# Optimization experiments

Measured on AMD Instinct MI355X. Metric: run time of the kernel, lower is better.

The kernel has to match this reference:

```python
import jax, jax.numpy as jnp
import numpy as np

N = 50000      # nodes
E = 800000     # directed edges (avg degree 16)
M = 10000      # hyperedges
P = 200000     # hypergraph incidence pairs (~4 per vertex)
D_IN = 64
D_OUT = 64
NEG_SLOPE = 0.2


def setup_inputs() -> dict:
    key = jax.random.key(0)
    ks = jax.random.split(key, 9)
    X = jax.random.normal(ks[0], (N, D_IN), jnp.float32)
    theta_w = jax.random.normal(ks[1], (D_OUT, D_IN), jnp.float32) / np.float32(np.sqrt(D_IN))
    theta_b = jax.random.normal(ks[2], (D_OUT,), jnp.float32) * 0.01
    a_src = jax.random.normal(ks[3], (D_OUT,), jnp.float32) / np.float32(np.sqrt(D_OUT))
    a_dst = jax.random.normal(ks[4], (D_OUT,), jnp.float32) / np.float32(np.sqrt(D_OUT))
    e_src = jax.random.randint(ks[5], (E,), 0, N, jnp.int32)
    e_dst = jax.random.randint(ks[6], (E,), 0, N, jnp.int32)
    inc_v = jax.random.randint(ks[7], (P,), 0, N, jnp.int32)
    inc_e = jax.random.randint(ks[8], (P,), 0, M, jnp.int32)
    return {"X": X, "theta_w": theta_w, "theta_b": theta_b, "a_src": a_src,
            "a_dst": a_dst, "e_src": e_src, "e_dst": e_dst,
            "inc_v": inc_v, "inc_e": inc_e}


def reference(X, theta_w, theta_b, a_src, a_dst, e_src, e_dst, inc_v, inc_e):
    # theta: Linear(in, out)
    Xp = X @ theta_w.T + theta_b                      # [N, D_OUT]
    # atten_src/atten_dst: Linear(out, 1, bias=False) -> per-node scalars
    s_src = Xp @ a_src                                # [N]
    s_dst = Xp @ a_dst                                # [N]
    # edge attention scores: gather + leaky_relu (dropout = identity in eval)
    score = jax.nn.leaky_relu(s_src[e_src] + s_dst[e_dst], NEG_SLOPE)  # [E]
    # segment softmax over incoming edges of each destination node
    seg_max = jax.ops.segment_max(score, e_dst, num_segments=N)
    seg_max = jax.lax.stop_gradient(jnp.where(jnp.isfinite(seg_max), seg_max, 0.0))
    w = jnp.exp(score - seg_max[e_dst])               # [E]
    denom = jax.ops.segment_sum(w, e_dst, num_segments=N)
    w = w / denom[e_dst]
    # weighted scatter-sum of source features (g.v2v softmax_then_sum)
    X_g = jax.ops.segment_sum(w[:, None] * Xp[e_src], e_dst, num_segments=N)
    # HGNN smoothing: D_v^{-1/2} H D_e^{-1} H^T D_v^{-1/2} Xp  (unit hyperedge weights)
    ones_p = jnp.ones((P,), Xp.dtype)
    dv = jax.ops.segment_sum(ones_p, inc_v, num_segments=N)
    de = jax.ops.segment_sum(ones_p, inc_e, num_segments=M)
    dv_isqrt = jnp.where(dv > 0, jax.lax.rsqrt(jnp.maximum(dv, 1.0)), 0.0)
    de_inv = jnp.where(de > 0, 1.0 / jnp.maximum(de, 1.0), 0.0)
    Xs = Xp * dv_isqrt[:, None]                        # [N, D_OUT]
    He = jax.ops.segment_sum(Xs[inc_v], inc_e, num_segments=M) * de_inv[:, None]  # [M, D_OUT]
    X_hg = jax.ops.segment_sum(He[inc_e], inc_v, num_segments=N) * dv_isqrt[:, None]
    X1 = (X_g + X_hg) * 0.5
    return jax.nn.elu(X1)
```

## Files before the change

kernel.cpp:

```cpp
#include <hip/hip_runtime.h>
#include <math.h>

#define DD 64

typedef __attribute__((ext_vector_type(8))) short bf16x8;
typedef __attribute__((ext_vector_type(4))) float f32x4;

__device__ __forceinline__ unsigned short f2bf(float x) {
    unsigned int u = __float_as_uint(x);
    u += 0x7fffu + ((u >> 16) & 1u);
    return (unsigned short)(u >> 16);
}
__device__ __forceinline__ float bflo(unsigned int u) { return __uint_as_float(u << 16); }
__device__ __forceinline__ float bfhi(unsigned int u) { return __uint_as_float(u & 0xffff0000u); }

#define GEMM_BLOCKS 196

__global__ __launch_bounds__(256) void k_gemm_count(
    const float* __restrict__ X, const float* __restrict__ W,
    const float* __restrict__ bias, const float* __restrict__ a_src,
    const float* __restrict__ a_dst, unsigned short* __restrict__ Xp_bf,
    float* __restrict__ s_src, float* __restrict__ s_dst,
    const int* __restrict__ e_dst, const int* __restrict__ inc_e,
    const int* __restrict__ inc_v, int* __restrict__ hist_g,
    int* __restrict__ hist_ie, int* __restrict__ hist_iv,
    int N, int E, int P, int M)
{
    if (blockIdx.x >= GEMM_BLOCKS) {
        __shared__ int cnt[128];
        int b = blockIdx.x - GEMM_BLOCKS;
        const int* key; int n, B, SH, nblk, blk; int* hist;
        if (b < 256)      { key = e_dst; n = E; B = (N + 511) >> 9; SH = 9; nblk = 256; blk = b;       hist = hist_g;  }
        else if (b < 384) { key = inc_e; n = P; B = (M + 255) >> 8; SH = 8; nblk = 128; blk = b - 256; hist = hist_ie; }
        else              { key = inc_v; n = P; B = (N + 511) >> 9; SH = 9; nblk = 128; blk = b - 384; hist = hist_iv; }
        for (int i = threadIdx.x; i < B; i += 256) cnt[i] = 0;
        __syncthreads();
        int chunk = (n + nblk - 1) / nblk;
        int s = blk * chunk, e = min(n, s + chunk);
        for (int i = s + threadIdx.x; i < e; i += 256)
            atomicAdd(&cnt[key[i] >> SH], 1);
        __syncthreads();
        for (int i = threadIdx.x; i < B; i += 256)
            hist[i * nblk + blk] = cnt[i];
        return;
    }
    int t = threadIdx.x;
    int lane = t & 63;
    int col = lane & 15;
    int kq  = lane >> 4;
    int rowbase = kq * 4;

    bf16x8 bfrag[4][2];
    float bj[4], asr[4], adr[4];
    #pragma unroll
    for (int jt = 0; jt < 4; ++jt) {
        int j = jt * 16 + col;
        #pragma unroll
        for (int ks = 0; ks < 2; ++ks) {
            const float* wp = W + j * DD + ks * 32 + kq * 8;
            float4 w0 = *(const float4*)wp;
            float4 w1 = *(const float4*)(wp + 4);
            bf16x8 bb;
            bb[0] = (short)f2bf(w0.x); bb[1] = (short)f2bf(w0.y);
            bb[2] = (short)f2bf(w0.z); bb[3] = (short)f2bf(w0.w);
            bb[4] = (short)f2bf(w1.x); bb[5] = (short)f2bf(w1.y);
            bb[6] = (short)f2bf(w1.z); bb[7] = (short)f2bf(w1.w);
            bfrag[jt][ks] = bb;
        }
        bj[jt]  = bias[j];
        asr[jt] = a_src[j];
        adr[jt] = a_dst[j];
    }

    int wave  = (blockIdx.x * 256 + t) >> 6;
    int nwave = (GEMM_BLOCKS * 256) >> 6;
    int ntiles = (N + 15) >> 4;
    for (int tile = wave; tile < ntiles; tile += nwave) {
        int r0 = tile * 16;
        int rl = r0 + col;
        if (rl >= N) rl = N - 1;
        const float* xp = X + (size_t)rl * DD + kq * 8;
        float4 x0 = *(const float4*)xp;
        float4 x1 = *(const float4*)(xp + 4);
        float4 x2 = *(const float4*)(xp + 32);
        float4 x3 = *(const float4*)(xp + 36);
        bf16x8 a0, a1;
        a0[0] = (short)f2bf(x0.x); a0[1] = (short)f2bf(x0.y);
        a0[2] = (short)f2bf(x0.z); a0[3] = (short)f2bf(x0.w);
        a0[4] = (short)f2bf(x1.x); a0[5] = (short)f2bf(x1.y);
        a0[6] = (short)f2bf(x1.z); a0[7] = (short)f2bf(x1.w);
        a1[0] = (short)f2bf(x2.x); a1[1] = (short)f2bf(x2.y);
        a1[2] = (short)f2bf(x2.z); a1[3] = (short)f2bf(x2.w);
        a1[4] = (short)f2bf(x3.x); a1[5] = (short)f2bf(x3.y);
        a1[6] = (short)f2bf(x3.z); a1[7] = (short)f2bf(x3.w);

        f32x4 acc[4];
        #pragma unroll
        for (int jt = 0; jt < 4; ++jt) {
            f32x4 c = {bj[jt], bj[jt], bj[jt], bj[jt]};
            c = __builtin_amdgcn_mfma_f32_16x16x32_bf16(a0, bfrag[jt][0], c, 0, 0, 0);
            c = __builtin_amdgcn_mfma_f32_16x16x32_bf16(a1, bfrag[jt][1], c, 0, 0, 0);
            acc[jt] = c;
        }

        int orow = r0 + rowbase;
        #pragma unroll
        for (int jt = 0; jt < 4; ++jt) {
            #pragma unroll
            for (int r = 0; r < 4; ++r) {
                int rr = orow + r;
                if (rr < N)
                    Xp_bf[(size_t)rr * DD + jt * 16 + col] = f2bf(acc[jt][r]);
            }
        }

        float vs[4], vd[4];
        #pragma unroll
        for (int r = 0; r < 4; ++r) {
            vs[r] = acc[0][r] * asr[0] + acc[1][r] * asr[1]
                  + acc[2][r] * asr[2] + acc[3][r] * asr[3];
            vd[r] = acc[0][r] * adr[0] + acc[1][r] * adr[1]
                  + acc[2][r] * adr[2] + acc[3][r] * adr[3];
        }
        #pragma unroll
        for (int off = 1; off < 16; off <<= 1) {
            #pragma unroll
            for (int r = 0; r < 4; ++r) {
                vs[r] += __shfl_xor(vs[r], off, 64);
                vd[r] += __shfl_xor(vd[r], off, 64);
            }
        }
        if (col == 0) {
            #pragma unroll
            for (int r = 0; r < 4; ++r) {
                int rr = orow + r;
                if (rr < N) { s_src[rr] = vs[r]; s_dst[rr] = vd[r]; }
            }
        }
    }
}

__device__ void block_scan4(int* a, int len)
{
    __shared__ int wtot[16];
    __shared__ int carry_s;
    int tid = threadIdx.x, lane = tid & 63, wid = tid >> 6;
    if (tid == 0) carry_s = 0;
    __syncthreads();
    for (int base = 0; base < len; base += 4096) {
        int i0 = base + tid * 4;
        int v[4];
        #pragma unroll
        for (int k = 0; k < 4; ++k) { int i = i0 + k; v[k] = (i < len) ? a[i] : 0; }
        int s = v[0] + v[1] + v[2] + v[3];
        int incl = s;
        #pragma unroll
        for (int off = 1; off < 64; off <<= 1) {
            int t = __shfl_up(incl, off, 64);
            if (lane >= off) incl += t;
        }
        if (lane == 63) wtot[wid] = incl;
        __syncthreads();
        int carry = carry_s;
        int woff = 0;
        for (int wj = 0; wj < wid; ++wj) woff += wtot[wj];
        int excl = carry + woff + incl - s;
        int run = excl;
        #pragma unroll
        for (int k = 0; k < 4; ++k) { int i = i0 + k; if (i < len) a[i] = run; run += v[k]; }
        __syncthreads();
        if (tid == 1023) carry_s = run;
        __syncthreads();
    }
    if (tid == 0) a[len] = carry_s;
}

__global__ __launch_bounds__(1024) void k_scan3(
    int* h0, int l0, int* h1, int l1, int* h2, int l2)
{
    if (blockIdx.x == 0)      block_scan4(h0, l0);
    else if (blockIdx.x == 1) block_scan4(h1, l1);
    else                      block_scan4(h2, l2);
}

__global__ __launch_bounds__(256) void k_scat(
    const int* __restrict__ e_dst, const int* __restrict__ e_src,
    const int* __restrict__ inc_e, const int* __restrict__ inc_v,
    const int* __restrict__ hist_g, const int* __restrict__ hist_ie,
    const int* __restrict__ hist_iv,
    unsigned int* __restrict__ pg, unsigned int* __restrict__ pie,
    unsigned int* __restrict__ piv,
    int E, int P, int N, int M)
{
    __shared__ int cur[128];
    int b = blockIdx.x;
    const int *key, *pay, *base; unsigned int* out;
    int n, B, SH, nblk, blk;
    if (b < 256)      { key = e_dst; pay = e_src; n = E; B = (N + 511) >> 9; SH = 9; nblk = 256; blk = b;       base = hist_g;  out = pg;  }
    else if (b < 384) { key = inc_e; pay = inc_v; n = P; B = (M + 255) >> 8; SH = 8; nblk = 128; blk = b - 256; base = hist_ie; out = pie; }
    else              { key = inc_v; pay = inc_e; n = P; B = (N + 511) >> 9; SH = 9; nblk = 128; blk = b - 384; base = hist_iv; out = piv; }
    for (int i = threadIdx.x; i < B; i += 256) cur[i] = base[i * nblk + blk];
    __syncthreads();
    int chunk = (n + nblk - 1) / nblk;
    int s = blk * chunk, e = min(n, s + chunk);
    int mask = (1 << SH) - 1;
    for (int i = s + threadIdx.x; i < e; i += 256) {
        int k = key[i];
        int pos = atomicAdd(&cur[k >> SH], 1);
        out[pos] = (unsigned int)(k & mask) | ((unsigned int)pay[i] << SH);
    }
}

__global__ __launch_bounds__(256) void k_fine(
    const int* __restrict__ hist_g, const int* __restrict__ hist_ie,
    const int* __restrict__ hist_iv,
    const unsigned int* __restrict__ pg, const unsigned int* __restrict__ pie,
    const unsigned int* __restrict__ piv,
    int* __restrict__ src_sorted, int* __restrict__ v_sorted,
    int* __restrict__ e_sorted,
    int* __restrict__ start_g, int* __restrict__ start_e,
    int* __restrict__ start_v,
    float* __restrict__ dein, float* __restrict__ dvis, int N, int M)
{
    __shared__ int lh[513];
    __shared__ int lc[512];
    __shared__ int lwt[4];
    __shared__ int lout[10240];
    int Bg = (N + 511) >> 9, Bie = (M + 255) >> 8;
    int b = blockIdx.x, tid = threadIdx.x;
    const int* base; const unsigned int* pr; int* outp; int* startp; float* inv;
    int K, nblk, b0, NK, mode;
    if (b < Bg)            { base = hist_g;  pr = pg;  outp = src_sorted; startp = start_g; inv = nullptr; K = 512; nblk = 256; b0 = b;            NK = N; mode = 0; }
    else if (b < Bg + Bie) { base = hist_ie; pr = pie; outp = v_sorted;   startp = start_e; inv = dein;    K = 256; nblk = 128; b0 = b - Bg;       NK = M; mode = 2; }
    else                   { base = hist_iv; pr = piv; outp = e_sorted;   startp = start_v; inv = dvis;    K = 512; nblk = 128; b0 = b - Bg - Bie; NK = N; mode = 1; }
    int SHF = (K == 512) ? 9 : 8;

    int pbase = base[b0 * nblk], pend = base[(b0 + 1) * nblk];
    int cnt = pend - pbase;
    for (int i = tid; i < K; i += 256) { lh[i] = 0; lc[i] = 0; }
    __syncthreads();
    for (int i = tid; i < cnt; i += 256)
        atomicAdd(&lh[pr[pbase + i] & (K - 1)], 1);
    __syncthreads();

    int per = K >> 8;
    int i0 = tid * per;
    int a0 = lh[i0], a1 = (per == 2) ? lh[i0 + 1] : 0;
    int ssum = a0 + a1;
    int lane = tid & 63, wid = tid >> 6;
    int incl = ssum;
    #pragma unroll
    for (int off = 1; off < 64; off <<= 1) {
        int t = __shfl_up(incl, off, 64);
        if (lane >= off) incl += t;
    }
    if (lane == 63) lwt[wid] = incl;
    __syncthreads();
    int woff = 0;
    for (int wj = 0; wj < wid; ++wj) woff += lwt[wj];
    int excl = woff + incl - ssum;
    lh[i0] = excl;
    if (per == 2) lh[i0 + 1] = excl + a0;
    if (tid == 255) lh[K] = excl + ssum;
    __syncthreads();

    for (int i = tid; i < cnt; i += 256) {
        unsigned int q = pr[pbase + i];
        int kl = q & (K - 1);
        int pos = lh[kl] + atomicAdd(&lc[kl], 1);
        lout[pos < 10240 ? pos : 10239] = (int)(q >> SHF);
    }
    __syncthreads();
    for (int i = tid; i < cnt; i += 256)
        outp[pbase + i] = lout[i];
    for (int k = tid; k < K; k += 256) {
        int node = b0 * K + k;
        if (node < NK) {
            startp[node] = pbase + lh[k];
            if (mode) {
                int d = lh[k + 1] - lh[k];
                inv[node] = d > 0 ? (mode == 1 ? rsqrtf((float)d) : 1.0f / (float)d) : 0.0f;
            }
        }
    }
    int Bj = (NK + K - 1) / K;
    if (tid == 0 && b0 == Bj - 1) startp[NK] = pend;
}

__global__ __launch_bounds__(256, 4) void k_he(
    const int* __restrict__ start_e, const int* __restrict__ v_sorted,
    const unsigned short* __restrict__ Xp_bf, const float* __restrict__ dvis,
    const float* __restrict__ dein, unsigned short* __restrict__ He_bf, int M)
{
    __shared__ int   s_v[4][64];
    __shared__ float s_d[4][64];
    int lane = threadIdx.x & 63, grp = lane >> 3, gl = lane & 7;
    int wv = threadIdx.x >> 6;
    int e = (blockIdx.x * 256 + threadIdx.x) >> 6;
    if (e >= M) return;
    int s = start_e[e], t = start_e[e + 1];
    float a[8] = {0.f, 0.f, 0.f, 0.f, 0.f, 0.f, 0.f, 0.f};
    for (int base = s; base < t; base += 64) {
        int cnt = min(64, t - base);
        int v = 0; float dv = 0.f;
        if (lane < cnt) { v = v_sorted[base + lane]; dv = dvis[v]; }
        s_v[wv][lane] = v;
        s_d[wv][lane] = dv;
        int nIter = (cnt + 7) >> 3;
        int k = 0;
        for (; k + 1 < nIter; k += 2) {
            int i0 = grp + 8 * k, i1 = i0 + 8;
            int v0 = s_v[wv][i0];      int v1 = s_v[wv][i1];
            float d0 = s_d[wv][i0];    float d1 = s_d[wv][i1];
            uint4 r0 = *(const uint4*)(Xp_bf + (size_t)v0 * DD + gl * 8);
            uint4 r1 = *(const uint4*)(Xp_bf + (size_t)v1 * DD + gl * 8);
            a[0] = fmaf(d0, bflo(r0.x), a[0]); a[1] = fmaf(d0, bfhi(r0.x), a[1]);
            a[2] = fmaf(d0, bflo(r0.y), a[2]); a[3] = fmaf(d0, bfhi(r0.y), a[3]);
            a[4] = fmaf(d0, bflo(r0.z), a[4]); a[5] = fmaf(d0, bfhi(r0.z), a[5]);
            a[6] = fmaf(d0, bflo(r0.w), a[6]); a[7] = fmaf(d0, bfhi(r0.w), a[7]);
            a[0] = fmaf(d1, bflo(r1.x), a[0]); a[1] = fmaf(d1, bfhi(r1.x), a[1]);
            a[2] = fmaf(d1, bflo(r1.y), a[2]); a[3] = fmaf(d1, bfhi(r1.y), a[3]);
            a[4] = fmaf(d1, bflo(r1.z), a[4]); a[5] = fmaf(d1, bfhi(r1.z), a[5]);
            a[6] = fmaf(d1, bflo(r1.w), a[6]); a[7] = fmaf(d1, bfhi(r1.w), a[7]);
        }
        if (k < nIter) {
            int i0 = grp + 8 * k;
            int v0 = s_v[wv][i0];
            float d0 = s_d[wv][i0];
            uint4 r0 = *(const uint4*)(Xp_bf + (size_t)v0 * DD + gl * 8);
            a[0] = fmaf(d0, bflo(r0.x), a[0]); a[1] = fmaf(d0, bfhi(r0.x), a[1]);
            a[2] = fmaf(d0, bflo(r0.y), a[2]); a[3] = fmaf(d0, bfhi(r0.y), a[3]);
            a[4] = fmaf(d0, bflo(r0.z), a[4]); a[5] = fmaf(d0, bfhi(r0.z), a[5]);
            a[6] = fmaf(d0, bflo(r0.w), a[6]); a[7] = fmaf(d0, bfhi(r0.w), a[7]);
        }
    }
    #pragma unroll
    for (int off = 8; off < 64; off <<= 1) {
        #pragma unroll
        for (int j = 0; j < 8; ++j) a[j] += __shfl_xor(a[j], off, 64);
    }
    if (grp == 0) {
        float din = dein[e];
        uint4 o;
        o.x = (unsigned)f2bf(a[0] * din) | ((unsigned)f2bf(a[1] * din) << 16);
        o.y = (unsigned)f2bf(a[2] * din) | ((unsigned)f2bf(a[3] * din) << 16);
        o.z = (unsigned)f2bf(a[4] * din) | ((unsigned)f2bf(a[5] * din) << 16);
        o.w = (unsigned)f2bf(a[6] * din) | ((unsigned)f2bf(a[7] * din) << 16);
        *(uint4*)(He_bf + (size_t)e * DD + gl * 8) = o;
    }
}

__global__ __launch_bounds__(256, 4) void k_out(
    const int* __restrict__ start_g, const int* __restrict__ src_sorted,
    const int* __restrict__ start_v, const int* __restrict__ e_sorted,
    const float* __restrict__ ssrc, const float* __restrict__ sdst,
    const unsigned short* __restrict__ Xp_bf, const unsigned short* __restrict__ He_bf,
    const float* __restrict__ dvis, float* __restrict__ out, int N)
{
    __shared__ int   s_i[4][64];
    __shared__ float s_w[4][64];
    int lane = threadIdx.x & 63, grp = lane >> 3, gl = lane & 7;
    int wv = threadIdx.x >> 6;
    int n = (blockIdx.x * 256 + threadIdx.x) >> 6;
    if (n >= N) return;

    float sd = sdst[n];
    int gs = start_g[n], ge = start_g[n + 1];
    float g[8] = {0.f, 0.f, 0.f, 0.f, 0.f, 0.f, 0.f, 0.f};
    float wsum = 0.f;
    for (int base = gs; base < ge; base += 64) {
        int cnt = min(64, ge - base);
        int idx = 0; float w = 0.f;
        if (lane < cnt) {
            idx = src_sorted[base + lane];
            float sc = ssrc[idx] + sd;
            sc = sc > 0.f ? sc : 0.2f * sc;
            w = __expf(sc);
        }
        s_i[wv][lane] = idx;
        s_w[wv][lane] = w;
        wsum += w;
        int nIter = (cnt + 7) >> 3;
        int k = 0;
        for (; k + 1 < nIter; k += 2) {
            int i0 = grp + 8 * k, i1 = i0 + 8;
            int s0 = s_i[wv][i0];     int s1 = s_i[wv][i1];
            float w0 = s_w[wv][i0];   float w1 = s_w[wv][i1];
            uint4 r0 = *(const uint4*)(Xp_bf + (size_t)s0 * DD + gl * 8);
            uint4 r1 = *(const uint4*)(Xp_bf + (size_t)s1 * DD + gl * 8);
            g[0] = fmaf(w0, bflo(r0.x), g[0]); g[1] = fmaf(w0, bfhi(r0.x), g[1]);
            g[2] = fmaf(w0, bflo(r0.y), g[2]); g[3] = fmaf(w0, bfhi(r0.y), g[3]);
            g[4] = fmaf(w0, bflo(r0.z), g[4]); g[5] = fmaf(w0, bfhi(r0.z), g[5]);
            g[6] = fmaf(w0, bflo(r0.w), g[6]); g[7] = fmaf(w0, bfhi(r0.w), g[7]);
            g[0] = fmaf(w1, bflo(r1.x), g[0]); g[1] = fmaf(w1, bfhi(r1.x), g[1]);
            g[2] = fmaf(w1, bflo(r1.y), g[2]); g[3] = fmaf(w1, bfhi(r1.y), g[3]);
            g[4] = fmaf(w1, bflo(r1.z), g[4]); g[5] = fmaf(w1, bfhi(r1.z), g[5]);
            g[6] = fmaf(w1, bflo(r1.w), g[6]); g[7] = fmaf(w1, bfhi(r1.w), g[7]);
        }
        if (k < nIter) {
            int i0 = grp + 8 * k;
            int s0 = s_i[wv][i0];
            float w0 = s_w[wv][i0];
            uint4 r0 = *(const uint4*)(Xp_bf + (size_t)s0 * DD + gl * 8);
            g[0] = fmaf(w0, bflo(r0.x), g[0]); g[1] = fmaf(w0, bfhi(r0.x), g[1]);
            g[2] = fmaf(w0, bflo(r0.y), g[2]); g[3] = fmaf(w0, bfhi(r0.y), g[3]);
            g[4] = fmaf(w0, bflo(r0.z), g[4]); g[5] = fmaf(w0, bfhi(r0.z), g[5]);
            g[6] = fmaf(w0, bflo(r0.w), g[6]); g[7] = fmaf(w0, bfhi(r0.w), g[7]);
        }
    }

    int vs = start_v[n], ve = start_v[n + 1];
    float h[8] = {0.f, 0.f, 0.f, 0.f, 0.f, 0.f, 0.f, 0.f};
    for (int base = vs; base < ve; base += 64) {
        int cnt = min(64, ve - base);
        int eidx = 0; float hw = 0.f;
        if (lane < cnt) { eidx = e_sorted[base + lane]; hw = 1.f; }
        s_i[wv][lane] = eidx;
        s_w[wv][lane] = hw;
        int nIter = (cnt + 7) >> 3;
        int k = 0;
        for (; k + 1 < nIter; k += 2) {
            int i0 = grp + 8 * k, i1 = i0 + 8;
            int e0 = s_i[wv][i0];     int e1 = s_i[wv][i1];
            float m0 = s_w[wv][i0];   float m1 = s_w[wv][i1];
            uint4 r0 = *(const uint4*)(He_bf + (size_t)e0 * DD + gl * 8);
            uint4 r1 = *(const uint4*)(He_bf + (size_t)e1 * DD + gl * 8);
            h[0] = fmaf(m0, bflo(r0.x), h[0]); h[1] = fmaf(m0, bfhi(r0.x), h[1]);
            h[2] = fmaf(m0, bflo(r0.y), h[2]); h[3] = fmaf(m0, bfhi(r0.y), h[3]);
            h[4] = fmaf(m0, bflo(r0.z), h[4]); h[5] = fmaf(m0, bfhi(r0.z), h[5]);
            h[6] = fmaf(m0, bflo(r0.w), h[6]); h[7] = fmaf(m0, bfhi(r0.w), h[7]);
            h[0] = fmaf(m1, bflo(r1.x), h[0]); h[1] = fmaf(m1, bfhi(r1.x), h[1]);
            h[2] = fmaf(m1, bflo(r1.y), h[2]); h[3] = fmaf(m1, bfhi(r1.y), h[3]);
            h[4] = fmaf(m1, bflo(r1.z), h[4]); h[5] = fmaf(m1, bfhi(r1.z), h[5]);
            h[6] = fmaf(m1, bflo(r1.w), h[6]); h[7] = fmaf(m1, bfhi(r1.w), h[7]);
        }
        if (k < nIter) {
            int i0 = grp + 8 * k;
            int e0 = s_i[wv][i0];
            float m0 = s_w[wv][i0];
            uint4 r0 = *(const uint4*)(He_bf + (size_t)e0 * DD + gl * 8);
            h[0] = fmaf(m0, bflo(r0.x), h[0]); h[1] = fmaf(m0, bfhi(r0.x), h[1]);
            h[2] = fmaf(m0, bflo(r0.y), h[2]); h[3] = fmaf(m0, bfhi(r0.y), h[3]);
            h[4] = fmaf(m0, bflo(r0.z), h[4]); h[5] = fmaf(m0, bfhi(r0.z), h[5]);
            h[6] = fmaf(m0, bflo(r0.w), h[6]); h[7] = fmaf(m0, bfhi(r0.w), h[7]);
        }
    }

    #pragma unroll
    for (int off = 1; off < 8; off <<= 1)
        wsum += __shfl_xor(wsum, off, 64);
    #pragma unroll
    for (int off = 8; off < 64; off <<= 1) {
        #pragma unroll
        for (int j = 0; j < 8; ++j) {
            g[j] += __shfl_xor(g[j], off, 64);
            h[j] += __shfl_xor(h[j], off, 64);
        }
        wsum += __shfl_xor(wsum, off, 64);
    }
    if (grp == 0) {
        float winv = (ge > gs) ? 1.0f / wsum : 0.f;
        float dvn = dvis[n];
        float o[8];
        #pragma unroll
        for (int j = 0; j < 8; ++j) {
            float x = 0.5f * (g[j] * winv + dvn * h[j]);
            o[j] = x > 0.f ? x : expm1f(x);
        }
        float* op = out + (size_t)n * DD + gl * 8;
        *(float4*)op       = make_float4(o[0], o[1], o[2], o[3]);
        *(float4*)(op + 4) = make_float4(o[4], o[5], o[6], o[7]);
    }
}

extern "C" void kernel_launch(void* const* d_in, const int* in_sizes, int n_in,
                              void* d_out, int out_size, void* d_ws, size_t ws_size,
                              hipStream_t stream)
{
    const float* X     = (const float*)d_in[0];
    const float* W     = (const float*)d_in[1];
    const float* bias  = (const float*)d_in[2];
    const float* a_src = (const float*)d_in[3];
    const float* a_dst = (const float*)d_in[4];
    const int* e_src   = (const int*)d_in[5];
    const int* e_dst   = (const int*)d_in[6];
    const int* inc_v   = (const int*)d_in[7];
    const int* inc_e   = (const int*)d_in[8];
    float* out = (float*)d_out;

    const int N = in_sizes[0] / DD;
    const int E = in_sizes[5];
    const int P = in_sizes[7];
    const int M = 10000;
    const int Bg = (N + 511) >> 9, Bie = (M + 255) >> 8, Biv = Bg;

    char* p = (char*)d_ws;
    unsigned short* Xp_bf = (unsigned short*)p; p += (size_t)N * DD * 2;
    unsigned short* He_bf = (unsigned short*)p; p += (size_t)M * DD * 2;
    unsigned int* pg  = (unsigned int*)p; p += (size_t)E * 4;
    unsigned int* pie = (unsigned int*)p; p += (size_t)P * 4;
    unsigned int* piv = (unsigned int*)p; p += (size_t)P * 4;
    int* src_sorted = (int*)p; p += (size_t)E * 4;
    int* v_sorted   = (int*)p; p += (size_t)P * 4;
    int* e_sorted   = (int*)p; p += (size_t)P * 4;
    float* ssrc = (float*)p; p += (size_t)N * 4;
    float* sdst = (float*)p; p += (size_t)N * 4;
    float* dvis = (float*)p; p += (size_t)N * 4;
    float* dein = (float*)p; p += (size_t)M * 4;
    int* start_g = (int*)p; p += (size_t)(N + 1) * 4;
    int* start_v = (int*)p; p += (size_t)(N + 1) * 4;
    int* start_e = (int*)p; p += (size_t)(M + 1) * 4;
    int* hist_g  = (int*)p; p += (size_t)(Bg * 256 + 1) * 4;
    int* hist_ie = (int*)p; p += (size_t)(Bie * 128 + 1) * 4;
    int* hist_iv = (int*)p; p += (size_t)(Biv * 128 + 1) * 4;

    k_gemm_count<<<GEMM_BLOCKS + 512, 256, 0, stream>>>(
        X, W, bias, a_src, a_dst, Xp_bf, ssrc, sdst,
        e_dst, inc_e, inc_v, hist_g, hist_ie, hist_iv, N, E, P, M);
    k_scan3<<<3, 1024, 0, stream>>>(hist_g, Bg * 256, hist_ie, Bie * 128,
                                    hist_iv, Biv * 128);
    k_scat<<<512, 256, 0, stream>>>(e_dst, e_src, inc_e, inc_v,
                                    hist_g, hist_ie, hist_iv, pg, pie, piv,
                                    E, P, N, M);
    k_fine<<<Bg + Bie + Biv, 256, 0, stream>>>(hist_g, hist_ie, hist_iv, pg, pie, piv,
                                               src_sorted, v_sorted, e_sorted,
                                               start_g, start_e, start_v,
                                               dein, dvis, N, M);
    k_he<<<(M * DD + 255) / 256, 256, 0, stream>>>(start_e, v_sorted, Xp_bf, dvis,
                                                   dein, He_bf, M);
    k_out<<<(N * DD + 255) / 256, 256, 0, stream>>>(start_g, src_sorted, start_v,
                                                    e_sorted, ssrc, sdst, Xp_bf,
                                                    He_bf, dvis, out, N);
}
```

Before: 117.9 us.

## Remap gather lanes to two neighbors per step with 4-byte loads

In k_he and k_out, each wave now splits into two 32-lane halves. Each lane reads a 4-byte pair of bf16 features per neighbor, replacing the previous eight groups of 8 lanes reading 16-byte chunks. This cuts per-thread accumulators from 8 to 2 and reduces the cross-lane reduction to a single shuffle, and launch bounds rise to allow 8 blocks per SM. In exchange, each wave walks neighbor lists in steps of two instead of eight. That lengthens the serial loop and raises the number of smaller memory transactions.

```diff
diff --git a/kernel.cpp b/kernel.cpp
--- a/kernel.cpp
+++ b/kernel.cpp
@@ -287,70 +287,53 @@
     if (tid == 0 && b0 == Bj - 1) startp[NK] = pend;
 }
 
-__global__ __launch_bounds__(256, 4) void k_he(
+__global__ __launch_bounds__(256, 8) void k_he(
     const int* __restrict__ start_e, const int* __restrict__ v_sorted,
     const unsigned short* __restrict__ Xp_bf, const float* __restrict__ dvis,
     const float* __restrict__ dein, unsigned short* __restrict__ He_bf, int M)
 {
     __shared__ int   s_v[4][64];
     __shared__ float s_d[4][64];
-    int lane = threadIdx.x & 63, grp = lane >> 3, gl = lane & 7;
+    int lane = threadIdx.x & 63, half = lane >> 5, hl = lane & 31;
     int wv = threadIdx.x >> 6;
     int e = (blockIdx.x * 256 + threadIdx.x) >> 6;
     if (e >= M) return;
     int s = start_e[e], t = start_e[e + 1];
-    float a[8] = {0.f, 0.f, 0.f, 0.f, 0.f, 0.f, 0.f, 0.f};
+    float a0 = 0.f, a1 = 0.f;
     for (int base = s; base < t; base += 64) {
         int cnt = min(64, t - base);
         int v = 0; float dv = 0.f;
         if (lane < cnt) { v = v_sorted[base + lane]; dv = dvis[v]; }
         s_v[wv][lane] = v;
         s_d[wv][lane] = dv;
-        int nIter = (cnt + 7) >> 3;
+        int nPair = (cnt + 1) >> 1;
         int k = 0;
-        for (; k + 1 < nIter; k += 2) {
-            int i0 = grp + 8 * k, i1 = i0 + 8;
-            int v0 = s_v[wv][i0];      int v1 = s_v[wv][i1];
-            float d0 = s_d[wv][i0];    float d1 = s_d[wv][i1];
-            uint4 r0 = *(const uint4*)(Xp_bf + (size_t)v0 * DD + gl * 8);
-            uint4 r1 = *(const uint4*)(Xp_bf + (size_t)v1 * DD + gl * 8);
-            a[0] = fmaf(d0, bflo(r0.x), a[0]); a[1] = fmaf(d0, bfhi(r0.x), a[1]);
-            a[2] = fmaf(d0, bflo(r0.y), a[2]); a[3] = fmaf(d0, bfhi(r0.y), a[3]);
-            a[4] = fmaf(d0, bflo(r0.z), a[4]); a[5] = fmaf(d0, bfhi(r0.z), a[5]);
-            a[6] = fmaf(d0, bflo(r0.w), a[6]); a[7] = fmaf(d0, bfhi(r0.w), a[7]);
-            a[0] = fmaf(d1, bflo(r1.x), a[0]); a[1] = fmaf(d1, bfhi(r1.x), a[1]);
-            a[2] = fmaf(d1, bflo(r1.y), a[2]); a[3] = fmaf(d1, bfhi(r1.y), a[3]);
-            a[4] = fmaf(d1, bflo(r1.z), a[4]); a[5] = fmaf(d1, bfhi(r1.z), a[5]);
-            a[6] = fmaf(d1, bflo(r1.w), a[6]); a[7] = fmaf(d1, bfhi(r1.w), a[7]);
-        }
-        if (k < nIter) {
-            int i0 = grp + 8 * k;
-            int v0 = s_v[wv][i0];
-            float d0 = s_d[wv][i0];
-            uint4 r0 = *(const uint4*)(Xp_bf + (size_t)v0 * DD + gl * 8);
-            a[0] = fmaf(d0, bflo(r0.x), a[0]); a[1] = fmaf(d0, bfhi(r0.x), a[1]);
-            a[2] = fmaf(d0, bflo(r0.y), a[2]); a[3] = fmaf(d0, bfhi(r0.y), a[3]);
-            a[4] = fmaf(d0, bflo(r0.z), a[4]); a[5] = fmaf(d0, bfhi(r0.z), a[5]);
-            a[6] = fmaf(d0, bflo(r0.w), a[6]); a[7] = fmaf(d0, bfhi(r0.w), a[7]);
-        }
-    }
-    #pragma unroll
-    for (int off = 8; off < 64; off <<= 1) {
-        #pragma unroll
-        for (int j = 0; j < 8; ++j) a[j] += __shfl_xor(a[j], off, 64);
-    }
-    if (grp == 0) {
+        for (; k + 1 < nPair; k += 2) {
+            int i0 = 2 * k + half, i1 = i0 + 2;
+            int v0 = s_v[wv][i0]; float d0 = s_d[wv][i0];
+            int v1 = s_v[wv][i1]; float d1 = s_d[wv][i1];
+            unsigned r0 = *(const unsigned*)(Xp_bf + (size_t)v0 * DD + hl * 2);
+            unsigned r1 = *(const unsigned*)(Xp_bf + (size_t)v1 * DD + hl * 2);
+            a0 = fmaf(d0, bflo(r0), a0); a1 = fmaf(d0, bfhi(r0), a1);
+            a0 = fmaf(d1, bflo(r1), a0); a1 = fmaf(d1, bfhi(r1), a1);
+        }
+        if (k < nPair) {
+            int i0 = 2 * k + half;
+            int v0 = s_v[wv][i0]; float d0 = s_d[wv][i0];
+            unsigned r0 = *(const unsigned*)(Xp_bf + (size_t)v0 * DD + hl * 2);
+            a0 = fmaf(d0, bflo(r0), a0); a1 = fmaf(d0, bfhi(r0), a1);
+        }
+    }
+    a0 += __shfl_xor(a0, 32, 64);
+    a1 += __shfl_xor(a1, 32, 64);
+    if (half == 0) {
         float din = dein[e];
-        uint4 o;
-        o.x = (unsigned)f2bf(a[0] * din) | ((unsigned)f2bf(a[1] * din) << 16);
-        o.y = (unsigned)f2bf(a[2] * din) | ((unsigned)f2bf(a[3] * din) << 16);
-        o.z = (unsigned)f2bf(a[4] * din) | ((unsigned)f2bf(a[5] * din) << 16);
-        o.w = (unsigned)f2bf(a[6] * din) | ((unsigned)f2bf(a[7] * din) << 16);
-        *(uint4*)(He_bf + (size_t)e * DD + gl * 8) = o;
-    }
-}
-
-__global__ __launch_bounds__(256, 4) void k_out(
+        unsigned o = (unsigned)f2bf(a0 * din) | ((unsigned)f2bf(a1 * din) << 16);
+        *(unsigned*)(He_bf + (size_t)e * DD + hl * 2) = o;
+    }
+}
+
+__global__ __launch_bounds__(256, 8) void k_out(
     const int* __restrict__ start_g, const int* __restrict__ src_sorted,
     const int* __restrict__ start_v, const int* __restrict__ e_sorted,
     const float* __restrict__ ssrc, const float* __restrict__ sdst,
@@ -359,15 +342,14 @@
 {
     __shared__ int   s_i[4][64];
     __shared__ float s_w[4][64];
-    int lane = threadIdx.x & 63, grp = lane >> 3, gl = lane & 7;
+    int lane = threadIdx.x & 63, half = lane >> 5, hl = lane & 31;
     int wv = threadIdx.x >> 6;
     int n = (blockIdx.x * 256 + threadIdx.x) >> 6;
     if (n >= N) return;
 
     float sd = sdst[n];
     int gs = start_g[n], ge = start_g[n + 1];
-    float g[8] = {0.f, 0.f, 0.f, 0.f, 0.f, 0.f, 0.f, 0.f};
-    float wsum = 0.f;
+    float g0 = 0.f, g1 = 0.f, wsum = 0.f;
     for (int base = gs; base < ge; base += 64) {
         int cnt = min(64, ge - base);
         int idx = 0; float w = 0.f;
@@ -380,96 +362,68 @@
         s_i[wv][lane] = idx;
         s_w[wv][lane] = w;
         wsum += w;
-        int nIter = (cnt + 7) >> 3;
+        int nPair = (cnt + 1) >> 1;
         int k = 0;
-        for (; k + 1 < nIter; k += 2) {
-            int i0 = grp + 8 * k, i1 = i0 + 8;
-            int s0 = s_i[wv][i0];     int s1 = s_i[wv][i1];
-            float w0 = s_w[wv][i0];   float w1 = s_w[wv][i1];
-            uint4 r0 = *(const uint4*)(Xp_bf + (size_t)s0 * DD + gl * 8);
-            uint4 r1 = *(const uint4*)(Xp_bf + (size_t)s1 * DD + gl * 8);
-            g[0] = fmaf(w0, bflo(r0.x), g[0]); g[1] = fmaf(w0, bfhi(r0.x), g[1]);
-            g[2] = fmaf(w0, bflo(r0.y), g[2]); g[3] = fmaf(w0, bfhi(r0.y), g[3]);
-            g[4] = fmaf(w0, bflo(r0.z), g[4]); g[5] = fmaf(w0, bfhi(r0.z), g[5]);
-            g[6] = fmaf(w0, bflo(r0.w), g[6]); g[7] = fmaf(w0, bfhi(r0.w), g[7]);
-            g[0] = fmaf(w1, bflo(r1.x), g[0]); g[1] = fmaf(w1, bfhi(r1.x), g[1]);
-            g[2] = fmaf(w1, bflo(r1.y), g[2]); g[3] = fmaf(w1, bfhi(r1.y), g[3]);
-            g[4] = fmaf(w1, bflo(r1.z), g[4]); g[5] = fmaf(w1, bfhi(r1.z), g[5]);
-            g[6] = fmaf(w1, bflo(r1.w), g[6]); g[7] = fmaf(w1, bfhi(r1.w), g[7]);
-        }
-        if (k < nIter) {
-            int i0 = grp + 8 * k;
-            int s0 = s_i[wv][i0];
-            float w0 = s_w[wv][i0];
-            uint4 r0 = *(const uint4*)(Xp_bf + (size_t)s0 * DD + gl * 8);
-            g[0] = fmaf(w0, bflo(r0.x), g[0]); g[1] = fmaf(w0, bfhi(r0.x), g[1]);
-            g[2] = fmaf(w0, bflo(r0.y), g[2]); g[3] = fmaf(w0, bfhi(r0.y), g[3]);
-            g[4] = fmaf(w0, bflo(r0.z), g[4]); g[5] = fmaf(w0, bfhi(r0.z), g[5]);
-            g[6] = fmaf(w0, bflo(r0.w), g[6]); g[7] = fmaf(w0, bfhi(r0.w), g[7]);
+        for (; k + 1 < nPair; k += 2) {
+            int i0 = 2 * k + half, i1 = i0 + 2;
+            int s0 = s_i[wv][i0]; float w0 = s_w[wv][i0];
+            int s1 = s_i[wv][i1]; float w1 = s_w[wv][i1];
+            unsigned r0 = *(const unsigned*)(Xp_bf + (size_t)s0 * DD + hl * 2);
+            unsigned r1 = *(const unsigned*)(Xp_bf + (size_t)s1 * DD + hl * 2);
+            g0 = fmaf(w0, bflo(r0), g0); g1 = fmaf(w0, bfhi(r0), g1);
+            g0 = fmaf(w1, bflo(r1), g0); g1 = fmaf(w1, bfhi(r1), g1);
+        }
+        if (k < nPair) {
+            int i0 = 2 * k + half;
+            int s0 = s_i[wv][i0]; float w0 = s_w[wv][i0];
+            unsigned r0 = *(const unsigned*)(Xp_bf + (size_t)s0 * DD + hl * 2);
+            g0 = fmaf(w0, bflo(r0), g0); g1 = fmaf(w0, bfhi(r0), g1);
         }
     }
 
     int vs = start_v[n], ve = start_v[n + 1];
-    float h[8] = {0.f, 0.f, 0.f, 0.f, 0.f, 0.f, 0.f, 0.f};
+    float h0 = 0.f, h1 = 0.f;
     for (int base = vs; base < ve; base += 64) {
         int cnt = min(64, ve - base);
         int eidx = 0; float hw = 0.f;
         if (lane < cnt) { eidx = e_sorted[base + lane]; hw = 1.f; }
         s_i[wv][lane] = eidx;
         s_w[wv][lane] = hw;
-        int nIter = (cnt + 7) >> 3;
+        int nPair = (cnt + 1) >> 1;
         int k = 0;
-        for (; k + 1 < nIter; k += 2) {
-            int i0 = grp + 8 * k, i1 = i0 + 8;
-            int e0 = s_i[wv][i0];     int e1 = s_i[wv][i1];
-            float m0 = s_w[wv][i0];   float m1 = s_w[wv][i1];
-            uint4 r0 = *(const uint4*)(He_bf + (size_t)e0 * DD + gl * 8);
-            uint4 r1 = *(const uint4*)(He_bf + (size_t)e1 * DD + gl * 8);
-            h[0] = fmaf(m0, bflo(r0.x), h[0]); h[1] = fmaf(m0, bfhi(r0.x), h[1]);
-            h[2] = fmaf(m0, bflo(r0.y), h[2]); h[3] = fmaf(m0, bfhi(r0.y), h[3]);
-            h[4] = fmaf(m0, bflo(r0.z), h[4]); h[5] = fmaf(m0, bfhi(r0.z), h[5]);
-            h[6] = fmaf(m0, bflo(r0.w), h[6]); h[7] = fmaf(m0, bfhi(r0.w), h[7]);
-            h[0] = fmaf(m1, bflo(r1.x), h[0]); h[1] = fmaf(m1, bfhi(r1.x), h[1]);
-            h[2] = fmaf(m1, bflo(r1.y), h[2]); h[3] = fmaf(m1, bfhi(r1.y), h[3]);
-            h[4] = fmaf(m1, bflo(r1.z), h[4]); h[5] = fmaf(m1, bfhi(r1.z), h[5]);
-            h[6] = fmaf(m1, bflo(r1.w), h[6]); h[7] = fmaf(m1, bfhi(r1.w), h[7]);
-        }
-        if (k < nIter) {
-            int i0 = grp + 8 * k;
-            int e0 = s_i[wv][i0];
-            float m0 = s_w[wv][i0];
-            uint4 r0 = *(const uint4*)(He_bf + (size_t)e0 * DD + gl * 8);
-            h[0] = fmaf(m0, bflo(r0.x), h[0]); h[1] = fmaf(m0, bfhi(r0.x), h[1]);
-            h[2] = fmaf(m0, bflo(r0.y), h[2]); h[3] = fmaf(m0, bfhi(r0.y), h[3]);
-            h[4] = fmaf(m0, bflo(r0.z), h[4]); h[5] = fmaf(m0, bfhi(r0.z), h[5]);
-            h[6] = fmaf(m0, bflo(r0.w), h[6]); h[7] = fmaf(m0, bfhi(r0.w), h[7]);
+        for (; k + 1 < nPair; k += 2) {
+            int i0 = 2 * k + half, i1 = i0 + 2;
+            int e0 = s_i[wv][i0]; float m0 = s_w[wv][i0];
+            int e1 = s_i[wv][i1]; float m1 = s_w[wv][i1];
+            unsigned r0 = *(const unsigned*)(He_bf + (size_t)e0 * DD + hl * 2);
+            unsigned r1 = *(const unsigned*)(He_bf + (size_t)e1 * DD + hl * 2);
+            h0 = fmaf(m0, bflo(r0), h0); h1 = fmaf(m0, bfhi(r0), h1);
+            h0 = fmaf(m1, bflo(r1), h0); h1 = fmaf(m1, bfhi(r1), h1);
+        }
+        if (k < nPair) {
+            int i0 = 2 * k + half;
+            int e0 = s_i[wv][i0]; float m0 = s_w[wv][i0];
+            unsigned r0 = *(const unsigned*)(He_bf + (size_t)e0 * DD + hl * 2);
+            h0 = fmaf(m0, bflo(r0), h0); h1 = fmaf(m0, bfhi(r0), h1);
         }
     }
 
     #pragma unroll
-    for (int off = 1; off < 8; off <<= 1)
+    for (int off = 1; off < 64; off <<= 1)
         wsum += __shfl_xor(wsum, off, 64);
-    #pragma unroll
-    for (int off = 8; off < 64; off <<= 1) {
-        #pragma unroll
-        for (int j = 0; j < 8; ++j) {
-            g[j] += __shfl_xor(g[j], off, 64);
-            h[j] += __shfl_xor(h[j], off, 64);
-        }
-        wsum += __shfl_xor(wsum, off, 64);
-    }
-    if (grp == 0) {
+    g0 += __shfl_xor(g0, 32, 64);
+    g1 += __shfl_xor(g1, 32, 64);
+    h0 += __shfl_xor(h0, 32, 64);
+    h1 += __shfl_xor(h1, 32, 64);
+
+    if (half == 0) {
         float winv = (ge > gs) ? 1.0f / wsum : 0.f;
         float dvn = dvis[n];
-        float o[8];
-        #pragma unroll
-        for (int j = 0; j < 8; ++j) {
-            float x = 0.5f * (g[j] * winv + dvn * h[j]);
-            o[j] = x > 0.f ? x : expm1f(x);
-        }
-        float* op = out + (size_t)n * DD + gl * 8;
-        *(float4*)op       = make_float4(o[0], o[1], o[2], o[3]);
-        *(float4*)(op + 4) = make_float4(o[4], o[5], o[6], o[7]);
+        float x0 = 0.5f * (g0 * winv + dvn * h0);
+        float x1 = 0.5f * (g1 * winv + dvn * h1);
+        x0 = x0 > 0.f ? x0 : expm1f(x0);
+        x1 = x1 > 0.f ? x1 : expm1f(x1);
+        *(float2*)(out + (size_t)n * DD + hl * 2) = make_float2(x0, x1);
     }
 }
 
```

Result: faster. 104.3 us (-11.5%).
